# Optimization experiments

Measured on AMD Instinct MI355X. Metric: run time of the kernel, lower is better.

## Reference

```python
import math
import jax, jax.numpy as jnp
import numpy as np

MODEL_DIM = 2048
INNER_DIM = 2048
NUM_HEADS = 32
NUM_BUCKETS = 32
MAX_DISTANCE = 128
B, S = 2, 2048


def _relative_position_buckets(q_len, k_len, num_buckets, max_distance):
    # bidirectional T5-style hybrid linear/log buckets
    qpos = jnp.arange(q_len, dtype=jnp.int32)[:, None]
    kpos = jnp.arange(k_len, dtype=jnp.int32)[None, :]
    dist = kpos - qpos  # [S, S]
    max_bucket = num_buckets // 2
    rel = (dist > 0).astype(jnp.int32) * max_bucket
    dist = jnp.abs(dist)
    limit = max_bucket // 2
    # log branch (clamp to >=1 to avoid log(0); masked out by where anyway)
    log_d = jnp.log(jnp.maximum(dist, 1).astype(jnp.float32) / limit)
    log_d = log_d / math.log(max_distance / limit) * (max_bucket - limit)
    log_d = limit + log_d.astype(jnp.int32)
    log_d = jnp.minimum(log_d, max_bucket - 1)
    rel = rel + jnp.where(dist < limit, dist, log_d)
    return rel  # [S, S] int32


def setup_inputs() -> dict:
    key = jax.random.key(0)
    ks = jax.random.split(key, 6)
    x = jax.random.normal(ks[0], (B, S, MODEL_DIM), dtype=jnp.float32)
    w_scale = 0.02
    wq = jax.random.normal(ks[1], (INNER_DIM, MODEL_DIM), dtype=jnp.float32) * w_scale
    wk = jax.random.normal(ks[2], (INNER_DIM, MODEL_DIM), dtype=jnp.float32) * w_scale
    wv = jax.random.normal(ks[3], (INNER_DIM, MODEL_DIM), dtype=jnp.float32) * w_scale
    wo = jax.random.normal(ks[4], (MODEL_DIM, INNER_DIM), dtype=jnp.float32) * w_scale
    rel_bias = jax.random.normal(ks[5], (NUM_BUCKETS, NUM_HEADS), dtype=jnp.float32) * 0.5
    return {"x": x, "wq": wq, "wk": wk, "wv": wv, "wo": wo, "rel_bias": rel_bias}


def reference(x, wq, wk, wv, wo, rel_bias):
    b, s, _ = x.shape
    h = NUM_HEADS
    hd = INNER_DIM // h
    buckets = _relative_position_buckets(s, s, NUM_BUCKETS, MAX_DISTANCE)  # [S,S]
    # embedding lookup then permute(2,0,1).unsqueeze(0) -> [1, H, S, S]
    position_bias = rel_bias[buckets].transpose(2, 0, 1)[None].astype(x.dtype)
    q = (x @ wq.T).reshape(b, s, h, hd)
    k = (x @ wk.T).reshape(b, s, h, hd)
    v = (x @ wv.T).reshape(b, s, h, hd)
    # scale = 1.0 (no 1/sqrt(head_dim))
    scores = jnp.einsum("bqhd,bkhd->bhqk", q, k) + position_bias
    attn = jax.nn.softmax(scores, axis=-1)
    ctx = jnp.einsum("bhqk,bkhd->bqhd", attn, v).reshape(b, s, INNER_DIM)
    out = ctx @ wo.T
    return (out, position_bias)
```

## Files before the change

### kernel.cpp

```cpp
#include <hip/hip_runtime.h>
#include <stdint.h>

typedef __bf16 bf16;
typedef __bf16 bf16x8 __attribute__((ext_vector_type(8)));
typedef __bf16 bf16x4 __attribute__((ext_vector_type(4)));
typedef float f32x4 __attribute__((ext_vector_type(4)));
typedef float f32x16 __attribute__((ext_vector_type(16)));
typedef unsigned int u32;

#define S 2048
#define DM 2048
#define NH 32
#define HD 64

#define GLDS16(g, l)                                                   \
  __builtin_amdgcn_global_load_lds(                                    \
      (const __attribute__((address_space(1))) void*)(g),              \
      (__attribute__((address_space(3))) void*)(l), 16, 0, 0)

__device__ __forceinline__ int bucket_of(int dist) {
  int rel = dist > 0 ? 16 : 0;
  int ad = dist < 0 ? -dist : dist;
  int b;
  if (ad < 8)       b = ad;
  else if (ad < 12) b = 8;
  else if (ad < 16) b = 9;
  else if (ad < 23) b = 10;
  else if (ad < 32) b = 11;
  else if (ad < 46) b = 12;
  else if (ad < 64) b = 13;
  else if (ad < 91) b = 14;
  else              b = 15;
  return rel + b;
}

__global__ void bucket_kernel(int8_t* __restrict__ table) {
  int i = blockIdx.x * 256 + threadIdx.x;
  if (i < 4095) table[i] = (int8_t)bucket_of(i - 2047);
}

__global__ void cast6(const float* __restrict__ s0, const float* __restrict__ s1,
                      const float* __restrict__ s2, const float* __restrict__ s3,
                      const float* __restrict__ s4, const float* __restrict__ s5,
                      bf16* __restrict__ dst) {
  int seg = blockIdx.y;
  const float* src = seg == 0 ? s0 : seg == 1 ? s1 : seg == 2 ? s2
                   : seg == 3 ? s3 : seg == 4 ? s4 : s5;
  int i = blockIdx.x * 256 + threadIdx.x;
  float4 v = ((const float4*)src)[i];
  bf16x4 o;
  o[0] = (bf16)v.x; o[1] = (bf16)v.y; o[2] = (bf16)v.z; o[3] = (bf16)v.w;
  *(bf16x4*)(dst + (size_t)seg * DM * DM + (size_t)i * 4) = o;
}

__global__ void pb_kernel(const float* __restrict__ rel_bias,
                          const int8_t* __restrict__ table,
                          float* __restrict__ pb) {
  int q = blockIdx.x, h = blockIdx.y;
  __shared__ float bias_h[32];
  if (threadIdx.x < 32) bias_h[threadIdx.x] = rel_bias[threadIdx.x * NH + h];
  __syncthreads();
  int k0 = threadIdx.x * 8;
  const int8_t* tb = table + (2047 - q);
  float4 a, bq;
  a.x = bias_h[tb[k0 + 0]]; a.y = bias_h[tb[k0 + 1]];
  a.z = bias_h[tb[k0 + 2]]; a.w = bias_h[tb[k0 + 3]];
  bq.x = bias_h[tb[k0 + 4]]; bq.y = bias_h[tb[k0 + 5]];
  bq.z = bias_h[tb[k0 + 6]]; bq.w = bias_h[tb[k0 + 7]];
  float* row = pb + (size_t)h * S * S + (size_t)q * S + k0;
  *(float4*)row = a;
  *(float4*)(row + 4) = bq;
}

template <typename OutT>
__device__ __forceinline__ void gemm_body(const bf16* __restrict__ A,
                                          const bf16* __restrict__ W,
                                          OutT* __restrict__ C, int N, int K,
                                          int m0, int n0) {
  __shared__ bf16 As[128 * 32];
  __shared__ bf16 Ws[128 * 32];
  int t = threadIdx.x;
  int wave = t >> 6, lane = t & 63;
  int quad = lane >> 4, l16 = lane & 15;
  int wm = (wave >> 1) * 64, wn = (wave & 1) * 64;

  f32x4 zero = {0.f, 0.f, 0.f, 0.f};
  f32x4 acc[4][4];
  for (int i = 0; i < 4; i++)
    for (int j = 0; j < 4; j++) acc[i][j] = zero;

  int srow = wave * 32 + (lane >> 2);
  int scol = (lane & 3) * 8;
  const bf16* Ag = A + (size_t)(m0 + srow) * K + scol;
  const bf16* Wg = W + (size_t)(n0 + srow) * K + scol;
  bf16* AsBase = &As[(wave * 32) * 32];
  bf16* WsBase = &Ws[(wave * 32) * 32];

  for (int k0 = 0; k0 < K; k0 += 32) {
    __syncthreads();
    GLDS16(Ag + k0, AsBase);
    GLDS16(Ag + (size_t)16 * K + k0, AsBase + 16 * 32);
    GLDS16(Wg + k0, WsBase);
    GLDS16(Wg + (size_t)16 * K + k0, WsBase + 16 * 32);
    __syncthreads();
    bf16x8 af[4], wf[4];
    for (int i = 0; i < 4; i++)
      af[i] = *(const bf16x8*)&As[(wm + i * 16 + l16) * 32 + quad * 8];
    for (int j = 0; j < 4; j++)
      wf[j] = *(const bf16x8*)&Ws[(wn + j * 16 + l16) * 32 + quad * 8];
    for (int i = 0; i < 4; i++)
      for (int j = 0; j < 4; j++)
        acc[i][j] = __builtin_amdgcn_mfma_f32_16x16x32_bf16(af[i], wf[j],
                                                            acc[i][j], 0, 0, 0);
  }
  for (int i = 0; i < 4; i++)
    for (int j = 0; j < 4; j++) {
      int col = n0 + wn + j * 16 + l16;
      for (int r = 0; r < 4; r++) {
        int row = m0 + wm + i * 16 + quad * 4 + r;
        C[(size_t)row * N + col] = (OutT)acc[i][j][r];
      }
    }
}

__global__ __launch_bounds__(256, 2)
void gemm_qkv(const bf16* __restrict__ A, const bf16* __restrict__ W0,
              const bf16* __restrict__ W1, const bf16* __restrict__ W2,
              bf16* __restrict__ C) {
  const bf16* W = blockIdx.z == 0 ? W0 : (blockIdx.z == 1 ? W1 : W2);
  bf16* Cz = C + (size_t)blockIdx.z * (size_t)2 * S * DM;
  gemm_body<bf16>(A, W, Cz, DM, DM, blockIdx.y * 128, blockIdx.x * 128);
}

__global__ __launch_bounds__(256, 2)
void gemm_out(const bf16* __restrict__ A, const bf16* __restrict__ W,
              float* __restrict__ C) {
  gemm_body<float>(A, W, C, DM, DM, blockIdx.y * 128, blockIdx.x * 128);
}

__global__ void transpose_v(const bf16* __restrict__ V, bf16* __restrict__ Vt) {
  int s0 = blockIdx.x * 64, h = blockIdx.y, b = blockIdx.z;
  __shared__ bf16 tile[64][72];
  int t = threadIdx.x;
  int r = t >> 3, c = (t & 7) * 8;
  for (int half = 0; half < 2; half++) {
    int row = half * 32 + r;
    *(bf16x8*)&tile[row][c] =
        *(const bf16x8*)(V + ((size_t)(b * S + s0 + row)) * DM + h * HD + c);
  }
  __syncthreads();
  int d = t >> 2, sc = (t & 3) * 16;
  for (int half = 0; half < 2; half++) {
    bf16x8 o;
    for (int j = 0; j < 8; j++) o[j] = tile[sc + half * 8 + j][d];
    *(bf16x8*)(Vt + ((size_t)((b * NH + h) * HD + d)) * S + s0 + sc + half * 8) = o;
  }
}

__global__ __launch_bounds__(256, 4)
void attn_kernel(const bf16* __restrict__ Q, const bf16* __restrict__ K,
                 const bf16* __restrict__ Vt, const float* __restrict__ rel_bias,
                 const int8_t* __restrict__ table, bf16* __restrict__ ctx_out) {
  int q0 = blockIdx.x * 128;
  int h = blockIdx.y, b = blockIdx.z;
  int t = threadIdx.x;
  int wave = t >> 6, lane = t & 63;
  int l31 = lane & 31, hi = lane >> 5;

  __shared__ bf16 Ks[128 * 72];
  __shared__ bf16 Vs[64 * 136];
  __shared__ float bias_s[32];
  __shared__ uint8_t tab_s[4096];

  if (t < 32) bias_s[t] = rel_bias[t * NH + h];
  for (int i = t; i < 4095; i += 256) tab_s[i] = (uint8_t)table[i];

  int q = q0 + wave * 32 + l31;
  const bf16* qp = Q + ((size_t)(b * S + q)) * DM + h * HD + hi * 8;
  bf16x8 bq[4];
  for (int ds = 0; ds < 4; ds++) bq[ds] = *(const bf16x8*)(qp + ds * 16);

  f32x16 ctx[2];
  for (int i = 0; i < 16; i++) { ctx[0][i] = 0.f; ctx[1][i] = 0.f; }
  float l_run = 1e-30f;

  int kr = t >> 1, kc = (t & 1) * 32;
  int vr = t >> 2, vc = (t & 3) * 32;
  const bf16* Kg = K + ((size_t)(b * S + kr)) * DM + h * HD + kc;
  const bf16* Vg = Vt + ((size_t)((b * NH + h) * HD + vr)) * S + vc;

  for (int k0 = 0; k0 < S; k0 += 128) {
    __syncthreads();
    {
      const bf16* kp = Kg + (size_t)k0 * DM;
      bf16* kd = &Ks[kr * 72 + kc];
      *(bf16x8*)(kd)      = *(const bf16x8*)(kp);
      *(bf16x8*)(kd + 8)  = *(const bf16x8*)(kp + 8);
      *(bf16x8*)(kd + 16) = *(const bf16x8*)(kp + 16);
      *(bf16x8*)(kd + 24) = *(const bf16x8*)(kp + 24);
      const bf16* vp = Vg + k0;
      bf16* vd = &Vs[vr * 136 + vc];
      *(bf16x8*)(vd)      = *(const bf16x8*)(vp);
      *(bf16x8*)(vd + 8)  = *(const bf16x8*)(vp + 8);
      *(bf16x8*)(vd + 16) = *(const bf16x8*)(vp + 16);
      *(bf16x8*)(vd + 24) = *(const bf16x8*)(vp + 24);
    }
    __syncthreads();

    int dmax = k0 + 127 - q0, dmin = k0 - (q0 + 127);
    bool cflat = (dmax <= -91) || (dmin >= 91);
    float cshift = ((dmax <= -91) ? bias_s[15] : bias_s[31]) - 40.f;

    for (int kt = 0; kt < 4; kt++) {
      f32x16 sc;
      for (int i = 0; i < 16; i++) sc[i] = 0.f;
      int krb = (kt * 32 + l31) * 72 + hi * 8;
      for (int ds = 0; ds < 4; ds++) {
        bf16x8 ak = *(const bf16x8*)&Ks[krb + ds * 16];
        sc = __builtin_amdgcn_mfma_f32_32x32x16_bf16(ak, bq[ds], sc, 0, 0, 0);
      }
      int keyb = k0 + kt * 32 + 4 * hi - q + 2047;
      u32 ua[4], ub[4];
      for (int g = 0; g < 4; g++) {
        float p[4];
        for (int r = 0; r < 4; r++) {
          float v = sc[g * 4 + r];
          if (cflat) p[r] = __expf(v + cshift);
          else       p[r] = __expf(v + bias_s[tab_s[keyb + 8 * g + r]] - 40.f);
          l_run += p[r];
        }
        union { bf16x4 v4; u32 w[2]; } pk;
        pk.v4[0] = (bf16)p[0]; pk.v4[1] = (bf16)p[1];
        pk.v4[2] = (bf16)p[2]; pk.v4[3] = (bf16)p[3];
        ua[g] = pk.w[0]; ub[g] = pk.w[1];
      }
      for (int c = 0; c < 2; c++) {
        u32 ka = hi ? ua[2 * c + 1] : ua[2 * c];
        u32 kb = hi ? ub[2 * c + 1] : ub[2 * c];
        u32 sa = hi ? ua[2 * c]     : ua[2 * c + 1];
        u32 sb = hi ? ub[2 * c]     : ub[2 * c + 1];
        u32 ra = (u32)__shfl_xor((int)sa, 32, 64);
        u32 rb = (u32)__shfl_xor((int)sb, 32, 64);
        union { u32 w[4]; bf16x8 v; } pf;
        pf.w[0] = hi ? ra : ka;
        pf.w[1] = hi ? rb : kb;
        pf.w[2] = hi ? ka : ra;
        pf.w[3] = hi ? kb : rb;
        for (int dt = 0; dt < 2; dt++) {
          bf16x8 av = *(const bf16x8*)&Vs[(dt * 32 + l31) * 136 + kt * 32 +
                                          c * 16 + hi * 8];
          ctx[dt] =
              __builtin_amdgcn_mfma_f32_32x32x16_bf16(av, pf.v, ctx[dt], 0, 0, 0);
        }
      }
    }
  }

  l_run += __shfl_xor(l_run, 32, 64);
  float rl = 1.f / l_run;
  for (int dt = 0; dt < 2; dt++)
    for (int g = 0; g < 4; g++) {
      bf16x4 o;
      for (int r = 0; r < 4; r++) o[r] = (bf16)(ctx[dt][g * 4 + r] * rl);
      *(bf16x4*)&ctx_out[((size_t)(b * S + q)) * DM + h * HD + dt * 32 +
                         8 * g + 4 * hi] = o;
    }
}

extern "C" void kernel_launch(void* const* d_in, const int* in_sizes, int n_in,
                              void* d_out, int out_size, void* d_ws, size_t ws_size,
                              hipStream_t stream) {
  const float* x  = (const float*)d_in[0];
  const float* wq = (const float*)d_in[1];
  const float* wk = (const float*)d_in[2];
  const float* wv = (const float*)d_in[3];
  const float* wo = (const float*)d_in[4];
  const float* rb = (const float*)d_in[5];

  float* out = (float*)d_out;
  float* pb  = out + (size_t)2 * S * DM;

  const size_t PROJ = (size_t)2 * S * DM;
  const size_t WSZ  = (size_t)DM * DM;
  bf16* arena = (bf16*)pb;
  bf16* xb   = arena;
  bf16* wqb  = xb + PROJ;
  bf16* wkb  = wqb + WSZ;
  bf16* wvb  = wkb + WSZ;
  bf16* wob  = wvb + WSZ;
  bf16* qs   = wob + WSZ;
  bf16* ks   = qs + PROJ;
  bf16* vs   = ks + PROJ;
  bf16* ctxs = vs + PROJ;
  bf16* vts  = ctxs + PROJ;
  int8_t* table = (int8_t*)d_ws;

  bucket_kernel<<<16, 256, 0, stream>>>(table);

  cast6<<<dim3((int)(WSZ / 4) / 256, 6), 256, 0, stream>>>(
      x, x + WSZ, wq, wk, wv, wo, arena);

  gemm_qkv<<<dim3(DM / 128, (2 * S) / 128, 3), 256, 0, stream>>>(xb, wqb, wkb,
                                                                 wvb, qs);

  transpose_v<<<dim3(S / 64, NH, 2), 256, 0, stream>>>(vs, vts);

  attn_kernel<<<dim3(S / 128, NH, 2), 256, 0, stream>>>(qs, ks, vts, rb, table,
                                                        ctxs);

  gemm_out<<<dim3(DM / 128, (2 * S) / 128), 256, 0, stream>>>(ctxs, wob, out);

  pb_kernel<<<dim3(S, NH), 256, 0, stream>>>(rb, table, pb);
}
```

Before: 911.4 us.

## Load K/V tiles via global_load_lds with XOR-swizzled LDS layout and setprio

Replaces register-staged global-to-LDS copies of K and V tiles with direct global_load_lds 16-byte transfers. The padded layout is replaced by an XOR swizzle so LDS reads stay free of bank conflicts without padding. It also hoists the K fragment reads ahead of the MFMA chain and wraps the MFMAs in s_setprio to favour matrix issue. The goal is to cut VGPR use and instruction overhead on tile loads, with the risk that the swizzle indexing must match between writer and reader.

```diff
diff --git a/kernel.cpp b/kernel.cpp
--- a/kernel.cpp
+++ b/kernel.cpp
@@ -167,8 +167,8 @@
   int wave = t >> 6, lane = t & 63;
   int l31 = lane & 31, hi = lane >> 5;
 
-  __shared__ bf16 Ks[128 * 72];
-  __shared__ bf16 Vs[64 * 136];
+  __shared__ __align__(16) bf16 Ks[128 * 64];
+  __shared__ __align__(16) bf16 Vs[64 * 128];
   __shared__ float bias_s[32];
   __shared__ uint8_t tab_s[4096];
 
@@ -184,26 +184,24 @@
   for (int i = 0; i < 16; i++) { ctx[0][i] = 0.f; ctx[1][i] = 0.f; }
   float l_run = 1e-30f;
 
-  int kr = t >> 1, kc = (t & 1) * 32;
-  int vr = t >> 2, vc = (t & 3) * 32;
-  const bf16* Kg = K + ((size_t)(b * S + kr)) * DM + h * HD + kc;
-  const bf16* Vg = Vt + ((size_t)((b * NH + h) * HD + vr)) * S + vc;
+  int l3 = lane >> 3, l7 = lane & 7;
+  const bf16* Kg_row = K + ((size_t)(b * S + wave * 32 + l3)) * DM + h * HD +
+                       ((l7 ^ (l3 & 7)) * 8);
+  int l4 = lane >> 4, l15 = lane & 15;
+  const bf16* Vg_row =
+      Vt + ((size_t)((b * NH + h) * HD + wave * 16 + l4)) * S;
 
   for (int k0 = 0; k0 < S; k0 += 128) {
     __syncthreads();
-    {
-      const bf16* kp = Kg + (size_t)k0 * DM;
-      bf16* kd = &Ks[kr * 72 + kc];
-      *(bf16x8*)(kd)      = *(const bf16x8*)(kp);
-      *(bf16x8*)(kd + 8)  = *(const bf16x8*)(kp + 8);
-      *(bf16x8*)(kd + 16) = *(const bf16x8*)(kp + 16);
-      *(bf16x8*)(kd + 24) = *(const bf16x8*)(kp + 24);
-      const bf16* vp = Vg + k0;
-      bf16* vd = &Vs[vr * 136 + vc];
-      *(bf16x8*)(vd)      = *(const bf16x8*)(vp);
-      *(bf16x8*)(vd + 8)  = *(const bf16x8*)(vp + 8);
-      *(bf16x8*)(vd + 16) = *(const bf16x8*)(vp + 16);
-      *(bf16x8*)(vd + 24) = *(const bf16x8*)(vp + 24);
+#pragma unroll
+    for (int i = 0; i < 4; i++)
+      GLDS16(Kg_row + (size_t)(k0 + i * 8) * DM,
+             &Ks[(wave * 32 + i * 8) * 64]);
+#pragma unroll
+    for (int i = 0; i < 4; i++) {
+      int vx = (l15 ^ (i * 4 + l4)) * 8;
+      GLDS16(Vg_row + (size_t)(i * 4) * S + k0 + vx,
+             &Vs[(wave * 16 + i * 4) * 128]);
     }
     __syncthreads();
 
@@ -214,11 +212,16 @@
     for (int kt = 0; kt < 4; kt++) {
       f32x16 sc;
       for (int i = 0; i < 16; i++) sc[i] = 0.f;
-      int krb = (kt * 32 + l31) * 72 + hi * 8;
-      for (int ds = 0; ds < 4; ds++) {
-        bf16x8 ak = *(const bf16x8*)&Ks[krb + ds * 16];
-        sc = __builtin_amdgcn_mfma_f32_32x32x16_bf16(ak, bq[ds], sc, 0, 0, 0);
-      }
+      bf16x8 ak[4];
+#pragma unroll
+      for (int ds = 0; ds < 4; ds++)
+        ak[ds] = *(const bf16x8*)&Ks[(kt * 32 + l31) * 64 +
+                                     (((ds * 2 + hi) ^ (l31 & 7)) * 8)];
+      __builtin_amdgcn_s_setprio(1);
+#pragma unroll
+      for (int ds = 0; ds < 4; ds++)
+        sc = __builtin_amdgcn_mfma_f32_32x32x16_bf16(ak[ds], bq[ds], sc, 0, 0, 0);
+      __builtin_amdgcn_s_setprio(0);
       int keyb = k0 + kt * 32 + 4 * hi - q + 2047;
       u32 ua[4], ub[4];
       for (int g = 0; g < 4; g++) {
@@ -246,12 +249,13 @@
         pf.w[1] = hi ? rb : kb;
         pf.w[2] = hi ? ka : ra;
         pf.w[3] = hi ? kb : rb;
-        for (int dt = 0; dt < 2; dt++) {
-          bf16x8 av = *(const bf16x8*)&Vs[(dt * 32 + l31) * 136 + kt * 32 +
-                                          c * 16 + hi * 8];
-          ctx[dt] =
-              __builtin_amdgcn_mfma_f32_32x32x16_bf16(av, pf.v, ctx[dt], 0, 0, 0);
-        }
+        int vslot = ((kt * 4 + c * 2 + hi) ^ (l31 & 15)) * 8;
+        bf16x8 av0 = *(const bf16x8*)&Vs[(0 * 32 + l31) * 128 + vslot];
+        bf16x8 av1 = *(const bf16x8*)&Vs[(1 * 32 + l31) * 128 + vslot];
+        __builtin_amdgcn_s_setprio(1);
+        ctx[0] = __builtin_amdgcn_mfma_f32_32x32x16_bf16(av0, pf.v, ctx[0], 0, 0, 0);
+        ctx[1] = __builtin_amdgcn_mfma_f32_32x32x16_bf16(av1, pf.v, ctx[1], 0, 0, 0);
+        __builtin_amdgcn_s_setprio(0);
       }
     }
   }
```

Result: slower. 1.015 ms (+11.3%).
